# Performance work log

Measured on AMD Instinct MI355X. Metric: run time of the kernel, lower is better.

## Reference

```python
import jax, jax.numpy as jnp
import numpy as np

B, S, HID, NH, HD = 2, 8192, 768, 12, 64
BLOCK, NRAND = 64, 3


def _make_attn_indices():
    # Mirrors SparseSelfAttention.bigbird_attention index construction:
    # globals = first block + last block tokens; randoms = NRAND per block.
    rng = np.random.default_rng(0)
    glob = np.concatenate([np.arange(BLOCK), np.arange(S - BLOCK, S)])
    rand = [rng.permutation(BLOCK)[:NRAND] + i * BLOCK for i in range(S // BLOCK)]
    idx = np.unique(np.concatenate([glob] + rand))
    return jnp.asarray(idx, dtype=jnp.int32)


def setup_inputs() -> dict:
    key = jax.random.key(0)
    ks = jax.random.split(key, 6)
    w = lambda k: jax.random.normal(k, (HID, HID), jnp.float32) * 0.02
    return {
        "hidden_states": jax.random.normal(ks[0], (B, S, HID), jnp.float32),
        "attn_indices": _make_attn_indices(),
        "Wq": w(ks[1]), "bq": jnp.zeros((HID,), jnp.float32),
        "Wk": w(ks[2]), "bk": jnp.zeros((HID,), jnp.float32),
        "Wv": w(ks[3]), "bv": jnp.zeros((HID,), jnp.float32),
        "Wo": w(ks[4]), "bo": jnp.zeros((HID,), jnp.float32),
    }


def reference(hidden_states, attn_indices, Wq, bq, Wk, bk, Wv, bv, Wo, bo):
    # torch nn.Linear: y = x @ W.T + b
    heads = lambda x: x.reshape(B, S, NH, HD).transpose(0, 2, 1, 3)  # [B,H,S,d]
    q = heads(hidden_states @ Wq.T + bq)
    k = heads(hidden_states @ Wk.T + bk)
    v = heads(hidden_states @ Wv.T + bv)

    sel_q = q[:, :, attn_indices]  # gather selected queries [B,H,Nsel,d]
    scores = jnp.einsum('bhqd,bhkd->bhqk', sel_q, k) / jnp.sqrt(jnp.float32(HD))
    probs = jax.nn.softmax(scores, axis=-1)              # [B,H,Nsel,S]
    ctx = jnp.einsum('bhqk,bhkd->bhqd', probs, v)        # [B,H,Nsel,d]

    # scatter back into zeros (non-selected query positions stay zero)
    full = jnp.zeros_like(q).at[:, :, attn_indices].set(ctx)
    context = full.transpose(0, 2, 1, 3).reshape(B, S, HID)
    output = context @ Wo.T + bo
    return (output, probs)
```

## Files before the change

### kernel.cpp

```cpp
#include <hip/hip_runtime.h>
#include <hip/hip_bf16.h>

#define B_   2
#define S_   8192
#define HID_ 768
#define NH_  12
#define HD_  64

#define KC1 256
#define NC1 (S_ / KC1)
#define KC2 512
#define NC2 (S_ / KC2)

typedef __attribute__((ext_vector_type(8))) short short8;
typedef __attribute__((ext_vector_type(4))) float f32x4;

__device__ __forceinline__ ushort f2b(float x) {
    __hip_bfloat16 h = __float2bfloat16(x);
    return *reinterpret_cast<ushort*>(&h);
}

__device__ __forceinline__ int swzb(int row, int colbyte, int rowbytes) {
    return row * rowbytes + (colbyte ^ ((row & 7) << 4));
}

__device__ __forceinline__ void glds16(const ushort* g, ushort* l) {
    __builtin_amdgcn_global_load_lds(
        (__attribute__((address_space(1))) unsigned int*)g,
        (__attribute__((address_space(3))) unsigned int*)l, 16, 0, 0);
}

#define N4H (B_ * S_ * HID_ / 4)
#define N4W (HID_ * HID_ / 4)
__global__ void prep_kernel(const float* __restrict__ hidden, const float* __restrict__ bo,
                            const float* __restrict__ Wk, const float* __restrict__ Wv,
                            const float* __restrict__ Wq, const float* __restrict__ Wo,
                            ushort* __restrict__ Hb, float* __restrict__ out,
                            ushort* __restrict__ Wkb, ushort* __restrict__ Wvb,
                            ushort* __restrict__ Wqb, ushort* __restrict__ Wob) {
    const int total = 2 * N4H + 4 * N4W;
    for (int i = blockIdx.x * blockDim.x + threadIdx.x; i < total; i += gridDim.x * blockDim.x) {
        if (i < N4H) {
            float4 v = reinterpret_cast<const float4*>(hidden)[i];
            ushort4 o = {f2b(v.x), f2b(v.y), f2b(v.z), f2b(v.w)};
            reinterpret_cast<ushort4*>(Hb)[i] = o;
        } else if (i < 2 * N4H) {
            int j = i - N4H;
            reinterpret_cast<float4*>(out)[j] = reinterpret_cast<const float4*>(bo)[j % (HID_ / 4)];
        } else {
            int local = i - 2 * N4H;
            int which = local / N4W, j = local - which * N4W;
            const float* src = which == 0 ? Wk : (which == 1 ? Wv : (which == 2 ? Wq : Wo));
            ushort* dst = which == 0 ? Wkb : (which == 1 ? Wvb : (which == 2 ? Wqb : Wob));
            float sc = (which == 2) ? 0.125f : 1.0f;
            float4 v = reinterpret_cast<const float4*>(src)[j];
            ushort4 o = {f2b(v.x * sc), f2b(v.y * sc), f2b(v.z * sc), f2b(v.w * sc)};
            reinterpret_cast<ushort4*>(dst)[j] = o;
        }
    }
}

__global__ void gather_qb_kernel(const float* __restrict__ hidden, const int* __restrict__ idx,
                                 ushort* __restrict__ Qinb, int nq, int nqpad) {
    int m = blockIdx.x;
    int b = m / nqpad, qi = m - b * nqpad;
    int t = threadIdx.x;
    ushort4* dst = reinterpret_cast<ushort4*>(Qinb + (size_t)m * HID_);
    if (qi < nq) {
        int srow = b * S_ + idx[qi];
        const float4* src = reinterpret_cast<const float4*>(hidden + (size_t)srow * HID_);
        float4 a = src[t * 2], c = src[t * 2 + 1];
        ushort4 o0 = {f2b(a.x), f2b(a.y), f2b(a.z), f2b(a.w)};
        ushort4 o1 = {f2b(c.x), f2b(c.y), f2b(c.z), f2b(c.w)};
        dst[t * 2] = o0;
        dst[t * 2 + 1] = o1;
    } else {
        ushort4 z = {0, 0, 0, 0};
        dst[t * 2] = z;
        dst[t * 2 + 1] = z;
    }
}

__launch_bounds__(256)
__global__ void gemm_kv_kernel(const ushort* __restrict__ A,
                               const ushort* __restrict__ Wkb, const ushort* __restrict__ Wvb,
                               const float* __restrict__ bk, const float* __restrict__ bv,
                               ushort* __restrict__ Kb, ushort* __restrict__ Vt) {
    __shared__ __align__(16) ushort As[128 * 64];
    __shared__ __align__(16) ushort Ws[128 * 64];
    const int t = threadIdx.x;
    const int lane = t & 63, w = t >> 6;
    const int wr = w >> 1, wc = w & 1;
    const int m0 = blockIdx.x * 128;
    const bool isV = blockIdx.y >= 6;
    const int n0 = (isV ? (blockIdx.y - 6) : blockIdx.y) * 128;
    const ushort* W = isV ? Wvb : Wkb;
    const float* bias = isV ? bv : bk;

    f32x4 acc[4][4];
    #pragma unroll
    for (int i = 0; i < 4; ++i)
        #pragma unroll
        for (int j = 0; j < 4; ++j) acc[i][j] = (f32x4){0.f, 0.f, 0.f, 0.f};

    for (int k0 = 0; k0 < HID_; k0 += 64) {
        __syncthreads();
        #pragma unroll
        for (int it = 0; it < 4; ++it) {
            int sid = t + it * 256;
            int row = sid >> 3, seg = sid & 7;
            int cb = (seg * 16) ^ ((row & 7) << 4);
            glds16(A + (size_t)(m0 + row) * HID_ + k0 + cb / 2, (ushort*)((char*)As + sid * 16));
            glds16(W + (size_t)(n0 + row) * HID_ + k0 + cb / 2, (ushort*)((char*)Ws + sid * 16));
        }
        __syncthreads();

        short8 af[4][2], bf_[4][2];
        #pragma unroll
        for (int mi = 0; mi < 4; ++mi)
            #pragma unroll
            for (int kh = 0; kh < 2; ++kh)
                af[mi][kh] = *reinterpret_cast<const short8*>(
                    (char*)As + swzb(wr * 64 + mi * 16 + (lane & 15), (lane >> 4) * 16 + kh * 64, 128));
        #pragma unroll
        for (int ni = 0; ni < 4; ++ni)
            #pragma unroll
            for (int kh = 0; kh < 2; ++kh)
                bf_[ni][kh] = *reinterpret_cast<const short8*>(
                    (char*)Ws + swzb(wc * 64 + ni * 16 + (lane & 15), (lane >> 4) * 16 + kh * 64, 128));

        #pragma unroll
        for (int mi = 0; mi < 4; ++mi)
            #pragma unroll
            for (int ni = 0; ni < 4; ++ni) {
                acc[mi][ni] = __builtin_amdgcn_mfma_f32_16x16x32_bf16(af[mi][0], bf_[ni][0], acc[mi][ni], 0, 0, 0);
                acc[mi][ni] = __builtin_amdgcn_mfma_f32_16x16x32_bf16(af[mi][1], bf_[ni][1], acc[mi][ni], 0, 0, 0);
            }
    }

    float bl[4];
    #pragma unroll
    for (int ni = 0; ni < 4; ++ni)
        bl[ni] = bias[n0 + wc * 64 + ni * 16 + (lane & 15)];

    #pragma unroll
    for (int mi = 0; mi < 4; ++mi) {
        #pragma unroll
        for (int ni = 0; ni < 4; ++ni) {
            int n = n0 + wc * 64 + ni * 16 + (lane & 15);
            int h = n >> 6, d = n & 63;
            int s0 = m0 + wr * 64 + mi * 16 + (lane >> 4) * 4;
            if (isV) {
                int b = s0 >> 13, s = s0 & (S_ - 1);
                ushort4 o = {f2b(acc[mi][ni][0] + bl[ni]), f2b(acc[mi][ni][1] + bl[ni]),
                             f2b(acc[mi][ni][2] + bl[ni]), f2b(acc[mi][ni][3] + bl[ni])};
                *reinterpret_cast<ushort4*>(&Vt[((size_t)(b * NH_ + h) * HD_ + d) * S_ + s]) = o;
            } else {
                #pragma unroll
                for (int r = 0; r < 4; ++r) {
                    int m = s0 + r;
                    int b = m >> 13, s = m & (S_ - 1);
                    Kb[(((size_t)(b * NH_ + h)) * S_ + s) * HD_ + d] = f2b(acc[mi][ni][r] + bl[ni]);
                }
            }
        }
    }
}

enum { GST_PLAIN = 1, GST_SCATF32 = 2 };

template<int MODE>
__launch_bounds__(256)
__global__ void gemm_bf16_kernel(const ushort* __restrict__ A, const ushort* __restrict__ W,
                                 const float* __restrict__ bias, float bscale,
                                 ushort* __restrict__ C, float* __restrict__ Cf,
                                 const int* __restrict__ idx, int nq, int Mq) {
    __shared__ __align__(16) ushort As[128 * 64];
    __shared__ __align__(16) ushort Ws[128 * 64];
    const int t = threadIdx.x;
    const int lane = t & 63, w = t >> 6;
    const int wr = w >> 1, wc = w & 1;
    const int m0 = blockIdx.x * 128;
    const int n0 = blockIdx.y * 128;

    f32x4 acc[4][4];
    #pragma unroll
    for (int i = 0; i < 4; ++i)
        #pragma unroll
        for (int j = 0; j < 4; ++j) acc[i][j] = (f32x4){0.f, 0.f, 0.f, 0.f};

    for (int k0 = 0; k0 < HID_; k0 += 64) {
        __syncthreads();
        #pragma unroll
        for (int it = 0; it < 4; ++it) {
            int sid = t + it * 256;
            int row = sid >> 3, seg = sid & 7;
            int cb = (seg * 16) ^ ((row & 7) << 4);
            glds16(A + (size_t)(m0 + row) * HID_ + k0 + cb / 2, (ushort*)((char*)As + sid * 16));
            glds16(W + (size_t)(n0 + row) * HID_ + k0 + cb / 2, (ushort*)((char*)Ws + sid * 16));
        }
        __syncthreads();

        short8 af[4][2], bf_[4][2];
        #pragma unroll
        for (int mi = 0; mi < 4; ++mi)
            #pragma unroll
            for (int kh = 0; kh < 2; ++kh)
                af[mi][kh] = *reinterpret_cast<const short8*>(
                    (char*)As + swzb(wr * 64 + mi * 16 + (lane & 15), (lane >> 4) * 16 + kh * 64, 128));
        #pragma unroll
        for (int ni = 0; ni < 4; ++ni)
            #pragma unroll
            for (int kh = 0; kh < 2; ++kh)
                bf_[ni][kh] = *reinterpret_cast<const short8*>(
                    (char*)Ws + swzb(wc * 64 + ni * 16 + (lane & 15), (lane >> 4) * 16 + kh * 64, 128));

        #pragma unroll
        for (int mi = 0; mi < 4; ++mi)
            #pragma unroll
            for (int ni = 0; ni < 4; ++ni) {
                acc[mi][ni] = __builtin_amdgcn_mfma_f32_16x16x32_bf16(af[mi][0], bf_[ni][0], acc[mi][ni], 0, 0, 0);
                acc[mi][ni] = __builtin_amdgcn_mfma_f32_16x16x32_bf16(af[mi][1], bf_[ni][1], acc[mi][ni], 0, 0, 0);
            }
    }

    float bl[4];
    #pragma unroll
    for (int ni = 0; ni < 4; ++ni)
        bl[ni] = bias[n0 + wc * 64 + ni * 16 + (lane & 15)] * bscale;

    #pragma unroll
    for (int mi = 0; mi < 4; ++mi) {
        #pragma unroll
        for (int ni = 0; ni < 4; ++ni) {
            int n = n0 + wc * 64 + ni * 16 + (lane & 15);
            #pragma unroll
            for (int r = 0; r < 4; ++r) {
                int m = m0 + wr * 64 + mi * 16 + (lane >> 4) * 4 + r;
                float fv = acc[mi][ni][r] + bl[ni];
                if (MODE == GST_PLAIN) {
                    C[(size_t)m * HID_ + n] = f2b(fv);
                } else {
                    if (m < Mq) {
                        int b = m / nq, qi = m - b * nq;
                        int srow = b * S_ + idx[qi];
                        Cf[(size_t)srow * HID_ + n] = fv;
                    }
                }
            }
        }
    }
}

__launch_bounds__(512)
__global__ void attn_pass1_mfma(const ushort* __restrict__ Qsel, const ushort* __restrict__ Kb,
                                float2* __restrict__ mlp, int nq, int nqpad) {
    __shared__ __align__(16) ushort Ks[128 * 64];
    const int t = threadIdx.x;
    const int lane = t & 63, w = t >> 6;
    const int lin = blockIdx.x;
    const int chunk = lin & (NC1 - 1), bh = lin >> 5;
    const int b = bh / NH_, h = bh - b * NH_;
    const int nqt = nqpad >> 7;

    short8 qa[4][2];
    #pragma unroll
    for (int qt = 0; qt < 4; ++qt) {
        if (qt < nqt) {
            const ushort* qp = Qsel + (size_t)(b * nqpad + qt * 128 + 16 * w + (lane & 15)) * HID_
                               + h * HD_ + (lane >> 4) * 8;
            qa[qt][0] = *reinterpret_cast<const short8*>(qp);
            qa[qt][1] = *reinterpret_cast<const short8*>(qp + 32);
        }
    }

    float m_r[4][4], l_r[4][4];
    #pragma unroll
    for (int qt = 0; qt < 4; ++qt)
        #pragma unroll
        for (int r = 0; r < 4; ++r) { m_r[qt][r] = -1e30f; l_r[qt][r] = 0.f; }

    const ushort* kbase = Kb + (size_t)bh * S_ * HD_;

    for (int kb = 0; kb < KC1; kb += 128) {
        int k0 = chunk * KC1 + kb;
        __syncthreads();
        #pragma unroll
        for (int it = 0; it < 2; ++it) {
            int sid = t + it * 512;
            int row = sid >> 3, seg = sid & 7;
            int cb = (seg * 16) ^ ((row & 7) << 4);
            glds16(kbase + (size_t)(k0 + row) * HD_ + cb / 2, (ushort*)((char*)Ks + sid * 16));
        }
        __syncthreads();

        short8 kf[8][2];
        #pragma unroll
        for (int ns = 0; ns < 8; ++ns) {
            kf[ns][0] = *reinterpret_cast<const short8*>((char*)Ks + swzb(ns * 16 + (lane & 15), (lane >> 4) * 16, 128));
            kf[ns][1] = *reinterpret_cast<const short8*>((char*)Ks + swzb(ns * 16 + (lane & 15), (lane >> 4) * 16 + 64, 128));
        }

        #pragma unroll
        for (int qt = 0; qt < 4; ++qt) {
            if (qt >= nqt) continue;
            f32x4 sf[8];
            __builtin_amdgcn_s_setprio(1);
            #pragma unroll
            for (int ns = 0; ns < 8; ++ns) {
                f32x4 acc = {0.f, 0.f, 0.f, 0.f};
                acc = __builtin_amdgcn_mfma_f32_16x16x32_bf16(qa[qt][0], kf[ns][0], acc, 0, 0, 0);
                acc = __builtin_amdgcn_mfma_f32_16x16x32_bf16(qa[qt][1], kf[ns][1], acc, 0, 0, 0);
                sf[ns] = acc;
            }
            __builtin_amdgcn_s_setprio(0);
            #pragma unroll
            for (int r = 0; r < 4; ++r) {
                float bm = sf[0][r];
                #pragma unroll
                for (int ns = 1; ns < 8; ++ns) bm = fmaxf(bm, sf[ns][r]);
                float mn = fmaxf(m_r[qt][r], bm);
                float sum = 0.f;
                #pragma unroll
                for (int ns = 0; ns < 8; ++ns) sum += __expf(sf[ns][r] - mn);
                l_r[qt][r] = l_r[qt][r] * __expf(m_r[qt][r] - mn) + sum;
                m_r[qt][r] = mn;
            }
        }
    }

    #pragma unroll
    for (int qt = 0; qt < 4; ++qt) {
        if (qt >= nqt) continue;
        #pragma unroll
        for (int r = 0; r < 4; ++r) {
            float m = m_r[qt][r], l = l_r[qt][r];
            #pragma unroll
            for (int off = 1; off < 16; off <<= 1) {
                float om = __shfl_xor(m, off);
                float ol = __shfl_xor(l, off);
                float mn = fmaxf(m, om);
                l = l * __expf(m - mn) + ol * __expf(om - mn);
                m = mn;
            }
            if ((lane & 15) == 0) {
                int row = qt * 128 + 16 * w + 4 * (lane >> 4) + r;
                mlp[(size_t)chunk * (B_ * NH_ * nqpad) + (size_t)bh * nqpad + row] = make_float2(m, l);
            }
        }
    }
}

__global__ void ml_reduce_kernel(const float2* __restrict__ mlp, float2* __restrict__ ml, int nqpad) {
    int i = blockIdx.x * blockDim.x + threadIdx.x;
    int total = B_ * NH_ * nqpad;
    if (i >= total) return;
    float m = -1e30f, l = 0.f;
    #pragma unroll
    for (int c = 0; c < NC1; ++c) {
        float2 v = mlp[(size_t)c * total + i];
        float mn = fmaxf(m, v.x);
        l = l * __expf(m - mn) + v.y * __expf(v.x - mn);
        m = mn;
    }
    ml[i] = make_float2(m, l);
}

__launch_bounds__(512)
__global__ void attn_pass2_mfma(const ushort* __restrict__ Qsel, const ushort* __restrict__ Kb,
                                const ushort* __restrict__ Vtb, const float2* __restrict__ ml,
                                float* __restrict__ probs, float* __restrict__ ctxp, int nq, int nqpad) {
    __shared__ __align__(16) ushort Ks[128 * 64];
    __shared__ __align__(16) ushort Vs[64 * 128];
    __shared__ __align__(16) ushort Ps[128 * 128];
    __shared__ float mls[256], ils[256];
    const int t = threadIdx.x;
    const int lane = t & 63, w = t >> 6;
    const int lin = blockIdx.x;
    const int xcd = lin & 7, slot = lin >> 3;
    const int qhalf = slot & 1, pl = slot >> 1;
    const int pair = xcd * 48 + pl;
    const int chunk = pair & (NC2 - 1), bh = pair >> 4;
    const int b = bh / NH_, h = bh - b * NH_;
    const int nqt = nqpad >> 7;

    short8 qa[2][2];
    #pragma unroll
    for (int ql = 0; ql < 2; ++ql) {
        int qt = qhalf * 2 + ql;
        if (qt < nqt) {
            const ushort* qp = Qsel + (size_t)(b * nqpad + qt * 128 + 16 * w + (lane & 15)) * HID_
                               + h * HD_ + (lane >> 4) * 8;
            qa[ql][0] = *reinterpret_cast<const short8*>(qp);
            qa[ql][1] = *reinterpret_cast<const short8*>(qp + 32);
        }
    }

    if (t < 256) {
        int row = qhalf * 256 + t;
        if (row < nqpad) {
            float2 v = ml[(size_t)bh * nqpad + row];
            mls[t] = v.x;
            ils[t] = 1.f / v.y;
        }
    }

    const ushort* kbase  = Kb  + (size_t)bh * S_ * HD_;
    const ushort* vtbase = Vtb + (size_t)bh * HD_ * S_;
    const size_t prow0 = (size_t)bh * nq;

    f32x4 accc[2][4];
    #pragma unroll
    for (int ql = 0; ql < 2; ++ql)
        #pragma unroll
        for (int d = 0; d < 4; ++d) accc[ql][d] = (f32x4){0.f, 0.f, 0.f, 0.f};

    for (int kb = 0; kb < KC2; kb += 128) {
        int k0 = chunk * KC2 + kb;
        __syncthreads();
        #pragma unroll
        for (int it = 0; it < 2; ++it) {
            int sid = t + it * 512;
            int row = sid >> 3, seg = sid & 7;
            int cb = (seg * 16) ^ ((row & 7) << 4);
            glds16(kbase + (size_t)(k0 + row) * HD_ + cb / 2, (ushort*)((char*)Ks + sid * 16));
        }
        #pragma unroll
        for (int it = 0; it < 2; ++it) {
            int sid = t + it * 512;
            int row = sid >> 4, seg = sid & 15;
            int cb = (seg * 16) ^ ((row & 7) << 4);
            glds16(vtbase + (size_t)row * S_ + k0 + cb / 2, (ushort*)((char*)Vs + sid * 16));
        }
        __syncthreads();

        #pragma unroll
        for (int ql = 0; ql < 2; ++ql) {
            int qt = qhalf * 2 + ql;
            if (qt >= nqt) continue;
            float mrq[4], ilq[4];
            #pragma unroll
            for (int r = 0; r < 4; ++r) {
                int lrow = ql * 128 + 16 * w + 4 * (lane >> 4) + r;
                mrq[r] = mls[lrow];
                ilq[r] = ils[lrow];
            }
            __builtin_amdgcn_s_setprio(1);
            #pragma unroll
            for (int ns = 0; ns < 8; ++ns) {
                short8 b0 = *reinterpret_cast<const short8*>((char*)Ks + swzb(ns * 16 + (lane & 15), (lane >> 4) * 16, 128));
                short8 b1 = *reinterpret_cast<const short8*>((char*)Ks + swzb(ns * 16 + (lane & 15), (lane >> 4) * 16 + 64, 128));
                f32x4 acc = {0.f, 0.f, 0.f, 0.f};
                acc = __builtin_amdgcn_mfma_f32_16x16x32_bf16(qa[ql][0], b0, acc, 0, 0, 0);
                acc = __builtin_amdgcn_mfma_f32_16x16x32_bf16(qa[ql][1], b1, acc, 0, 0, 0);
                #pragma unroll
                for (int r = 0; r < 4; ++r) {
                    int rl = 16 * w + 4 * (lane >> 4) + r;
                    float p = __expf(acc[r] - mrq[r]) * ilq[r];
                    int qrow = qt * 128 + rl;
                    if (qrow < nq)
                        probs[(prow0 + qrow) * (size_t)S_ + k0 + ns * 16 + (lane & 15)] = p;
                    *reinterpret_cast<ushort*>((char*)Ps + swzb(rl, (ns * 16 + (lane & 15)) * 2, 256)) = f2b(p);
                }
            }
            short8 pa[4];
            #pragma unroll
            for (int ks = 0; ks < 4; ++ks)
                pa[ks] = *reinterpret_cast<const short8*>((char*)Ps + swzb(16 * w + (lane & 15), ks * 64 + (lane >> 4) * 16, 256));
            #pragma unroll
            for (int ds = 0; ds < 4; ++ds) {
                #pragma unroll
                for (int ks = 0; ks < 4; ++ks) {
                    short8 vb = *reinterpret_cast<const short8*>((char*)Vs + swzb(ds * 16 + (lane & 15), ks * 64 + (lane >> 4) * 16, 256));
                    accc[ql][ds] = __builtin_amdgcn_mfma_f32_16x16x32_bf16(pa[ks], vb, accc[ql][ds], 0, 0, 0);
                }
            }
            __builtin_amdgcn_s_setprio(0);
        }
    }

    float* dst = ctxp + (size_t)chunk * ((size_t)B_ * nq * HID_);
    #pragma unroll
    for (int ql = 0; ql < 2; ++ql) {
        int qt = qhalf * 2 + ql;
        if (qt >= nqt) continue;
        #pragma unroll
        for (int ds = 0; ds < 4; ++ds) {
            #pragma unroll
            for (int r = 0; r < 4; ++r) {
                int qrow = qt * 128 + 16 * w + 4 * (lane >> 4) + r;
                if (qrow < nq)
                    dst[(size_t)(b * nq + qrow) * HID_ + h * HD_ + ds * 16 + (lane & 15)] = accc[ql][ds][r];
            }
        }
    }
}

__global__ void ctx_reduce_kernel(const float* __restrict__ ctxp, ushort* __restrict__ ctxb, int Mq) {
    const int n4 = Mq * (HID_ / 4);
    const float4* src = reinterpret_cast<const float4*>(ctxp);
    ushort4* dst = reinterpret_cast<ushort4*>(ctxb);
    for (int i = blockIdx.x * blockDim.x + threadIdx.x; i < n4; i += gridDim.x * blockDim.x) {
        float4 s = make_float4(0.f, 0.f, 0.f, 0.f);
        #pragma unroll
        for (int c = 0; c < NC2; ++c) {
            float4 v = src[(size_t)c * n4 + i];
            s.x += v.x; s.y += v.y; s.z += v.z; s.w += v.w;
        }
        ushort4 o;
        o.x = f2b(s.x); o.y = f2b(s.y); o.z = f2b(s.z); o.w = f2b(s.w);
        dst[i] = o;
    }
}

extern "C" void kernel_launch(void* const* d_in, const int* in_sizes, int n_in,
                              void* d_out, int out_size, void* d_ws, size_t ws_size,
                              hipStream_t stream) {
    const float* hidden = (const float*)d_in[0];
    const int*   idx    = (const int*)d_in[1];
    const float* Wq = (const float*)d_in[2];
    const float* bq = (const float*)d_in[3];
    const float* Wk = (const float*)d_in[4];
    const float* bk = (const float*)d_in[5];
    const float* Wv = (const float*)d_in[6];
    const float* bv = (const float*)d_in[7];
    const float* Wo = (const float*)d_in[8];
    const float* bo = (const float*)d_in[9];
    const int nq = in_sizes[1];
    const int qt128 = (nq + 127) / 128;
    const int nqpad = qt128 * 128;
    const int Mq = B_ * nq;
    const int Mqp = B_ * nqpad;

    float* out   = (float*)d_out;
    float* probs = out + (size_t)B_ * S_ * HID_;

    char* ws = (char*)d_ws;
    const size_t kvN = (size_t)B_ * NH_ * S_ * HD_;
    ushort* Hb    = (ushort*)ws;                 ws += kvN * 2;
    ushort* K_buf = (ushort*)ws;                 ws += kvN * 2;
    ushort* Vt    = (ushort*)ws;                 ws += kvN * 2;
    ushort* Wkb   = (ushort*)ws;                 ws += (size_t)HID_ * HID_ * 2;
    ushort* Wvb   = (ushort*)ws;                 ws += (size_t)HID_ * HID_ * 2;
    ushort* Wqb   = (ushort*)ws;                 ws += (size_t)HID_ * HID_ * 2;
    ushort* Wob   = (ushort*)ws;                 ws += (size_t)HID_ * HID_ * 2;
    ushort* Qinb  = (ushort*)ws;                 ws += (size_t)Mqp * HID_ * 2;
    ushort* Qsel  = (ushort*)ws;                 ws += (size_t)Mqp * HID_ * 2;
    ushort* ctxb  = (ushort*)ws;                 ws += (size_t)Mqp * HID_ * 2;
    float*  ctxp  = (float*)ws;                  ws += (size_t)NC2 * Mq * HID_ * 4;
    float2* mlp   = (float2*)ws;                 ws += (size_t)NC1 * B_ * NH_ * nqpad * 8;
    float2* ml    = (float2*)ws;                 ws += (size_t)B_ * NH_ * nqpad * 8;

    prep_kernel<<<2048, 256, 0, stream>>>(hidden, bo, Wk, Wv, Wq, Wo,
                                          Hb, out, Wkb, Wvb, Wqb, Wob);
    gather_qb_kernel<<<Mqp, 96, 0, stream>>>(hidden, idx, Qinb, nq, nqpad);

    dim3 gKV(B_ * S_ / 128, 12);
    gemm_kv_kernel<<<gKV, 256, 0, stream>>>(Hb, Wkb, Wvb, bk, bv, K_buf, Vt);

    dim3 gQ(Mqp / 128, HID_ / 128);
    gemm_bf16_kernel<GST_PLAIN><<<gQ, 256, 0, stream>>>(Qinb, Wqb, bq, 0.125f, Qsel, nullptr, nullptr, 0, 0);

    attn_pass1_mfma<<<NC1 * B_ * NH_, 512, 0, stream>>>(Qsel, K_buf, mlp, nq, nqpad);

    int totalml = B_ * NH_ * nqpad;
    ml_reduce_kernel<<<(totalml + 255) / 256, 256, 0, stream>>>(mlp, ml, nqpad);

    attn_pass2_mfma<<<2 * NC2 * B_ * NH_, 512, 0, stream>>>(Qsel, K_buf, Vt, ml, probs, ctxp, nq, nqpad);

    ctx_reduce_kernel<<<1024, 256, 0, stream>>>(ctxp, ctxb, Mq);

    gemm_bf16_kernel<GST_SCATF32><<<gQ, 256, 0, stream>>>(ctxb, Wob, bo, 1.0f, nullptr, out, idx, nq, Mq);
}
```

Measured before the change: 299.9 us.

## Vectorize probs stores via LDS, fuse ml reduce into pass2, remap KV GEMM blocks

Probability writes in attention pass 2 are moved out of the MFMA fragment loop and instead read back from the LDS P tile and stored as contiguous float4 pairs, improving global write coalescing. The separate ml_reduce kernel is removed; pass 2 reduces the per-chunk max/sum partials itself, saving a launch and an intermediate buffer. The KV GEMM grid is flattened and remapped so consecutive blocks on an XCD share row tiles for better L2 reuse. Output probabilities now come from bf16-rounded values, reducing their precision.

```diff
diff --git a/kernel.cpp b/kernel.cpp
--- a/kernel.cpp
+++ b/kernel.cpp
@@ -18,6 +18,10 @@
 __device__ __forceinline__ ushort f2b(float x) {
     __hip_bfloat16 h = __float2bfloat16(x);
     return *reinterpret_cast<ushort*>(&h);
+}
+__device__ __forceinline__ float b2f(ushort u) {
+    unsigned v = (unsigned)u << 16;
+    return __int_as_float(v);
 }
 
 __device__ __forceinline__ int swzb(int row, int colbyte, int rowbytes) {
@@ -91,9 +95,12 @@
     const int t = threadIdx.x;
     const int lane = t & 63, w = t >> 6;
     const int wr = w >> 1, wc = w & 1;
-    const int m0 = blockIdx.x * 128;
-    const bool isV = blockIdx.y >= 6;
-    const int n0 = (isV ? (blockIdx.y - 6) : blockIdx.y) * 128;
+    const int lin = blockIdx.x;
+    const int xcd = lin & 7, s_ = lin >> 3;
+    const int m0 = (xcd * 16 + s_ / 12) * 128;
+    const int yi = s_ % 12;
+    const bool isV = yi >= 6;
+    const int n0 = (isV ? yi - 6 : yi) * 128;
     const ushort* W = isV ? Wvb : Wkb;
     const float* bias = isV ? bv : bk;
 
@@ -351,24 +358,9 @@
     }
 }
 
-__global__ void ml_reduce_kernel(const float2* __restrict__ mlp, float2* __restrict__ ml, int nqpad) {
-    int i = blockIdx.x * blockDim.x + threadIdx.x;
-    int total = B_ * NH_ * nqpad;
-    if (i >= total) return;
-    float m = -1e30f, l = 0.f;
-    #pragma unroll
-    for (int c = 0; c < NC1; ++c) {
-        float2 v = mlp[(size_t)c * total + i];
-        float mn = fmaxf(m, v.x);
-        l = l * __expf(m - mn) + v.y * __expf(v.x - mn);
-        m = mn;
-    }
-    ml[i] = make_float2(m, l);
-}
-
 __launch_bounds__(512)
 __global__ void attn_pass2_mfma(const ushort* __restrict__ Qsel, const ushort* __restrict__ Kb,
-                                const ushort* __restrict__ Vtb, const float2* __restrict__ ml,
+                                const ushort* __restrict__ Vtb, const float2* __restrict__ mlp,
                                 float* __restrict__ probs, float* __restrict__ ctxp, int nq, int nqpad) {
     __shared__ __align__(16) ushort Ks[128 * 64];
     __shared__ __align__(16) ushort Vs[64 * 128];
@@ -398,11 +390,19 @@
 
     if (t < 256) {
         int row = qhalf * 256 + t;
+        float m = -1e30f, l = 1.f;
         if (row < nqpad) {
-            float2 v = ml[(size_t)bh * nqpad + row];
-            mls[t] = v.x;
-            ils[t] = 1.f / v.y;
-        }
+            l = 0.f;
+            #pragma unroll 4
+            for (int c = 0; c < NC1; ++c) {
+                float2 v = mlp[(size_t)c * (B_ * NH_ * nqpad) + (size_t)bh * nqpad + row];
+                float mn = fmaxf(m, v.x);
+                l = l * __expf(m - mn) + v.y * __expf(v.x - mn);
+                m = mn;
+            }
+        }
+        mls[t] = m;
+        ils[t] = 1.f / l;
     }
 
     const ushort* kbase  = Kb  + (size_t)bh * S_ * HD_;
@@ -457,9 +457,6 @@
                 for (int r = 0; r < 4; ++r) {
                     int rl = 16 * w + 4 * (lane >> 4) + r;
                     float p = __expf(acc[r] - mrq[r]) * ilq[r];
-                    int qrow = qt * 128 + rl;
-                    if (qrow < nq)
-                        probs[(prow0 + qrow) * (size_t)S_ + k0 + ns * 16 + (lane & 15)] = p;
                     *reinterpret_cast<ushort*>((char*)Ps + swzb(rl, (ns * 16 + (lane & 15)) * 2, 256)) = f2b(p);
                 }
             }
@@ -476,6 +473,22 @@
                 }
             }
             __builtin_amdgcn_s_setprio(0);
+
+            #pragma unroll
+            for (int it = 0; it < 4; ++it) {
+                int sl = it * 64 + lane;
+                int rl = 16 * w + (sl >> 4);
+                int seg = sl & 15;
+                int qrow = qt * 128 + rl;
+                if (qrow < nq) {
+                    short8 pv = *reinterpret_cast<const short8*>((char*)Ps + swzb(rl, seg * 16, 256));
+                    float4 f0 = {b2f((ushort)pv[0]), b2f((ushort)pv[1]), b2f((ushort)pv[2]), b2f((ushort)pv[3])};
+                    float4 f1 = {b2f((ushort)pv[4]), b2f((ushort)pv[5]), b2f((ushort)pv[6]), b2f((ushort)pv[7])};
+                    float* gp = &probs[(prow0 + qrow) * (size_t)S_ + k0 + seg * 8];
+                    *reinterpret_cast<float4*>(gp) = f0;
+                    *reinterpret_cast<float4*>(gp + 4) = f1;
+                }
+            }
         }
     }
 
@@ -549,24 +562,18 @@
     ushort* ctxb  = (ushort*)ws;                 ws += (size_t)Mqp * HID_ * 2;
     float*  ctxp  = (float*)ws;                  ws += (size_t)NC2 * Mq * HID_ * 4;
     float2* mlp   = (float2*)ws;                 ws += (size_t)NC1 * B_ * NH_ * nqpad * 8;
-    float2* ml    = (float2*)ws;                 ws += (size_t)B_ * NH_ * nqpad * 8;
 
     prep_kernel<<<2048, 256, 0, stream>>>(hidden, bo, Wk, Wv, Wq, Wo,
                                           Hb, out, Wkb, Wvb, Wqb, Wob);
     gather_qb_kernel<<<Mqp, 96, 0, stream>>>(hidden, idx, Qinb, nq, nqpad);
 
-    dim3 gKV(B_ * S_ / 128, 12);
-    gemm_kv_kernel<<<gKV, 256, 0, stream>>>(Hb, Wkb, Wvb, bk, bv, K_buf, Vt);
+    gemm_kv_kernel<<<B_ * S_ / 128 * 12, 256, 0, stream>>>(Hb, Wkb, Wvb, bk, bv, K_buf, Vt);
 
     dim3 gQ(Mqp / 128, HID_ / 128);
     gemm_bf16_kernel<GST_PLAIN><<<gQ, 256, 0, stream>>>(Qinb, Wqb, bq, 0.125f, Qsel, nullptr, nullptr, 0, 0);
 
     attn_pass1_mfma<<<NC1 * B_ * NH_, 512, 0, stream>>>(Qsel, K_buf, mlp, nq, nqpad);
-
-    int totalml = B_ * NH_ * nqpad;
-    ml_reduce_kernel<<<(totalml + 255) / 256, 256, 0, stream>>>(mlp, ml, nqpad);
-
-    attn_pass2_mfma<<<2 * NC2 * B_ * NH_, 512, 0, stream>>>(Qsel, K_buf, Vt, ml, probs, ctxp, nq, nqpad);
+    attn_pass2_mfma<<<2 * NC2 * B_ * NH_, 512, 0, stream>>>(Qsel, K_buf, Vt, mlp, probs, ctxp, nq, nqpad);
 
     ctx_reduce_kernel<<<1024, 256, 0, stream>>>(ctxp, ctxb, Mq);
 
```

Result: slower. 313.7 us (+4.6%).
